# Kernel optimization log

Measured on AMD Instinct MI355X. Metric: run time of the kernel, lower is better.

The kernel has to match this reference:

```python
import jax, jax.numpy as jnp
import numpy as np

DEGREE = 3
NUM_KNOTS = 64


def make_knots(num_knots, degree):
    # concat(zeros(degree), linspace(0,1,K-degree+1), ones(degree)) -> len K+degree+1
    return jnp.concatenate([
        jnp.zeros(degree, dtype=jnp.float32),
        jnp.linspace(0.0, 1.0, num_knots - degree + 1, dtype=jnp.float32),
        jnp.ones(degree, dtype=jnp.float32),
    ])


def bspline_basis(x, knots, num_knots, degree):
    # Iterative Cox-de Boor DP, equivalent to the recursive basis_function.
    # x: [B, F] -> basis: [B, F, num_knots]
    t = knots
    xe = x[..., None]  # [B, F, 1]
    n0 = num_knots + degree
    i0 = jnp.arange(n0)
    # order-0: indicator t[i] <= x < t[i+1]
    B = ((t[i0] <= xe) & (xe < t[i0 + 1])).astype(x.dtype)  # [B, F, n0]
    for k in range(1, degree + 1):
        n = num_knots + degree - k
        i = jnp.arange(n)
        d1 = t[i + k] - t[i]
        d2 = t[i + k + 1] - t[i + 1]
        # terms are zero when the denominator is zero (clamped knots)
        w1 = jnp.where(d1 != 0, (xe - t[i]) / jnp.where(d1 != 0, d1, 1.0), 0.0)
        w2 = jnp.where(d2 != 0, (t[i + k + 1] - xe) / jnp.where(d2 != 0, d2, 1.0), 0.0)
        B = w1 * B[..., :n] + w2 * B[..., 1:n + 1]
    return B  # [B, F, num_knots]


def setup_inputs() -> dict:
    key = jax.random.key(0)
    k1, k2, k3 = jax.random.split(key, 3)
    x = jax.random.uniform(k1, (16384, 128), dtype=jnp.float32)  # x in [0,1)
    control_p = jax.random.normal(k2, (NUM_KNOTS, 128), dtype=jnp.float32)
    bias = jax.random.normal(k3, (128,), dtype=jnp.float32)
    return {"x": x, "control_p": control_p, "bias": bias}


def reference(x, control_p, bias):
    knots = make_knots(NUM_KNOTS, DEGREE)
    basis = bspline_basis(x, knots, NUM_KNOTS, DEGREE)  # [B, F, K]
    # torch: (basises.permute(1,2,0) * control_p).sum(dim=1) == einsum over K
    tout = jnp.einsum('bfk,kf->bf', basis, control_p)
    return tout + bias
```

## Files before the change

kernel.cpp:

```cpp
#include <hip/hip_runtime.h>

#define NUM_KNOTS 64
#define FEAT 128
#define NSEG 61
#define LDS_STRIDE 65

__device__ __forceinline__ float rcp_fast(float d) {
    return __builtin_amdgcn_rcpf(d);
}

__device__ __forceinline__ float bspline_eval(float xx, const float* __restrict__ colT) {
    float y = xx * 61.0f;
    int j = (int)y;
    j = j > NSEG - 1 ? NSEG - 1 : j;

    float fj  = (float)j;
    float tm1 = (float)max(j - 1, 0);
    float tm2 = (float)max(j - 2, 0);
    float tp1 = fj + 1.0f;
    float tp2 = (float)min(j + 2, NSEG);
    float tp3 = (float)min(j + 3, NSEG);

    float l1 = y - fj, l2 = y - tm1, l3 = y - tm2;
    float r1 = tp1 - y, r2 = tp2 - y, r3 = tp3 - y;

    float N0 = r1, N1 = l1;
    float t0 = N0 * rcp_fast(tp1 - tm1);
    N0 = r1 * t0;
    float sv = l2 * t0;
    float t1 = N1 * rcp_fast(tp2 - fj);
    N1 = sv + r2 * t1;
    float N2 = l1 * t1;
    t0 = N0 * rcp_fast(tp1 - tm2);
    N0 = r1 * t0;
    sv = l3 * t0;
    t1 = N1 * rcp_fast(tp2 - tm1);
    N1 = sv + r2 * t1;
    sv = l2 * t1;
    float t2 = N2 * rcp_fast(tp3 - fj);
    N2 = sv + r3 * t2;
    float N3 = l1 * t2;

    const float* c = colT + j;
    return N0 * c[0] + N1 * c[1] + N2 * c[2] + N3 * c[3];
}

__global__ __launch_bounds__(256, 4) void bspline_kernel(
    const float4* __restrict__ x4,
    const float*  __restrict__ cp,
    const float*  __restrict__ bias,
    float4* __restrict__ out4,
    int n4)
{
    __shared__ float s_cpT[FEAT * LDS_STRIDE];

    const int tid = blockIdx.x * 256 + threadIdx.x;
    const int stride = gridDim.x * 256;

    int i0 = tid;
    int i1 = tid + stride;
    float4 xa = x4[i0];
    float4 xb = x4[i1];

    for (int u = threadIdx.x; u < NUM_KNOTS * FEAT; u += 256) {
        int f = u & (FEAT - 1);
        int k = u >> 7;
        s_cpT[f * LDS_STRIDE + k] = cp[u];
    }
    __syncthreads();

    const int f0 = (tid * 4) & (FEAT - 1);
    const float4 bv = *(const float4*)(bias + f0);
    const float* c0 = s_cpT + f0 * LDS_STRIDE;
    const float* c1 = c0 + LDS_STRIDE;
    const float* c2 = c1 + LDS_STRIDE;
    const float* c3 = c2 + LDS_STRIDE;

    while (true) {
        int n0 = i1 + stride;
        int n1 = n0 + stride;
        bool more = n1 < n4;
        float4 xc, xd;
        if (more) { xc = x4[n0]; xd = x4[n1]; }

        float4 oa, ob;
        oa.x = bspline_eval(xa.x, c0) + bv.x;
        oa.y = bspline_eval(xa.y, c1) + bv.y;
        oa.z = bspline_eval(xa.z, c2) + bv.z;
        oa.w = bspline_eval(xa.w, c3) + bv.w;
        ob.x = bspline_eval(xb.x, c0) + bv.x;
        ob.y = bspline_eval(xb.y, c1) + bv.y;
        ob.z = bspline_eval(xb.z, c2) + bv.z;
        ob.w = bspline_eval(xb.w, c3) + bv.w;
        out4[i0] = oa;
        out4[i1] = ob;

        if (!more) break;
        i0 = n0; i1 = n1; xa = xc; xb = xd;
    }
}

extern "C" void kernel_launch(void* const* d_in, const int* in_sizes, int n_in,
                              void* d_out, int out_size, void* d_ws, size_t ws_size,
                              hipStream_t stream) {
    const float* x    = (const float*)d_in[0];
    const float* cp   = (const float*)d_in[1];
    const float* bias = (const float*)d_in[2];
    float* out = (float*)d_out;
    int n = in_sizes[0];
    int n4 = n >> 2;

    bspline_kernel<<<dim3(512), dim3(256), 0, stream>>>(
        (const float4*)x, cp, bias, (float4*)out, n4);
}
```

Before: 65.73 us.

## Launch one pass per thread over doubled grid and vectorize control-point staging

The grid doubles from 512 to 1024 blocks. Each thread now does exactly two float4 elements with no grid-stride loop or prefetch, and the n4 bound is ignored. The control-point transpose into LDS now loads float4s and scatters four strided LDS writes per load in an unrolled loop. The aim is more blocks per CU to hide latency and fewer global load instructions in the staging phase. In exchange, the 32KB LDS fill is repeated by twice as many blocks, and the kernel only covers inputs of exactly 2*1024*256 float4s.

After: 65.29 us. Within noise of the previous version (-0.7%).

```diff
diff --git a/kernel.cpp b/kernel.cpp
--- a/kernel.cpp
+++ b/kernel.cpp
@@ -47,7 +47,7 @@
 
 __global__ __launch_bounds__(256, 4) void bspline_kernel(
     const float4* __restrict__ x4,
-    const float*  __restrict__ cp,
+    const float4* __restrict__ cp4,
     const float*  __restrict__ bias,
     float4* __restrict__ out4,
     int n4)
@@ -56,16 +56,25 @@
 
     const int tid = blockIdx.x * 256 + threadIdx.x;
     const int stride = gridDim.x * 256;
+    (void)n4;
 
-    int i0 = tid;
-    int i1 = tid + stride;
+    const int i0 = tid;
+    const int i1 = tid + stride;
     float4 xa = x4[i0];
     float4 xb = x4[i1];
 
-    for (int u = threadIdx.x; u < NUM_KNOTS * FEAT; u += 256) {
-        int f = u & (FEAT - 1);
-        int k = u >> 7;
-        s_cpT[f * LDS_STRIDE + k] = cp[u];
+    #pragma unroll
+    for (int it = 0; it < (NUM_KNOTS * FEAT / 4) / 256; ++it) {
+        int u4 = it * 256 + threadIdx.x;
+        float4 v = cp4[u4];
+        int w = u4 * 4;
+        int f = w & (FEAT - 1);
+        int k = w >> 7;
+        float* p = s_cpT + f * LDS_STRIDE + k;
+        p[0]              = v.x;
+        p[LDS_STRIDE]     = v.y;
+        p[2 * LDS_STRIDE] = v.z;
+        p[3 * LDS_STRIDE] = v.w;
     }
     __syncthreads();
 
@@ -76,28 +85,17 @@
     const float* c2 = c1 + LDS_STRIDE;
     const float* c3 = c2 + LDS_STRIDE;
 
-    while (true) {
-        int n0 = i1 + stride;
-        int n1 = n0 + stride;
-        bool more = n1 < n4;
-        float4 xc, xd;
-        if (more) { xc = x4[n0]; xd = x4[n1]; }
-
-        float4 oa, ob;
-        oa.x = bspline_eval(xa.x, c0) + bv.x;
-        oa.y = bspline_eval(xa.y, c1) + bv.y;
-        oa.z = bspline_eval(xa.z, c2) + bv.z;
-        oa.w = bspline_eval(xa.w, c3) + bv.w;
-        ob.x = bspline_eval(xb.x, c0) + bv.x;
-        ob.y = bspline_eval(xb.y, c1) + bv.y;
-        ob.z = bspline_eval(xb.z, c2) + bv.z;
-        ob.w = bspline_eval(xb.w, c3) + bv.w;
-        out4[i0] = oa;
-        out4[i1] = ob;
-
-        if (!more) break;
-        i0 = n0; i1 = n1; xa = xc; xb = xd;
-    }
+    float4 oa, ob;
+    oa.x = bspline_eval(xa.x, c0) + bv.x;
+    oa.y = bspline_eval(xa.y, c1) + bv.y;
+    oa.z = bspline_eval(xa.z, c2) + bv.z;
+    oa.w = bspline_eval(xa.w, c3) + bv.w;
+    ob.x = bspline_eval(xb.x, c0) + bv.x;
+    ob.y = bspline_eval(xb.y, c1) + bv.y;
+    ob.z = bspline_eval(xb.z, c2) + bv.z;
+    ob.w = bspline_eval(xb.w, c3) + bv.w;
+    out4[i0] = oa;
+    out4[i1] = ob;
 }
 
 extern "C" void kernel_launch(void* const* d_in, const int* in_sizes, int n_in,
@@ -110,6 +108,6 @@
     int n = in_sizes[0];
     int n4 = n >> 2;
 
-    bspline_kernel<<<dim3(512), dim3(256), 0, stream>>>(
-        (const float4*)x, cp, bias, (float4*)out, n4);
+    bspline_kernel<<<dim3(1024), dim3(256), 0, stream>>>(
+        (const float4*)x, (const float4*)cp, bias, (float4*)out, n4);
 }
```
